# Kernel tuning notes

Measured on AMD Instinct MI355X. Metric: run time of the kernel, lower is better.

## Reference

```python
import jax, jax.numpy as jnp
import numpy as np

FORGET_BIAS = 1.0  # BasicLSTMCell default


def setup_inputs() -> dict:
    key = jax.random.key(0)
    k1, k2 = jax.random.split(key)
    B, T, F, H = 64, 128, 1024, 1024
    x = jax.random.normal(k1, (B, T, F), dtype=jnp.float32)
    # BasicLSTMCell kernel: [F + H, 4H], init uniform(-0.1, 0.1); bias zeros
    W = jax.random.uniform(k2, (F + H, 4 * H), dtype=jnp.float32, minval=-0.1, maxval=0.1)
    b = jnp.zeros((4 * H,), dtype=jnp.float32)
    return {"x": x, "W": W, "b": b}


def reference(x, W, b):
    # x: [B, T, F]; W: [F+H, 4H]; b: [4H]
    B, T, F = x.shape
    H = W.shape[1] // 4

    def step(carry, xt):
        c, h = carry  # [B, H] each
        z = jnp.concatenate([xt, h], axis=-1) @ W + b  # [B, 4H]
        i, j, f, o = jnp.split(z, 4, axis=-1)
        new_c = c * jax.nn.sigmoid(f + FORGET_BIAS) + jax.nn.sigmoid(i) * jnp.tanh(j)
        new_h = jnp.tanh(new_c) * jax.nn.sigmoid(o)
        return (new_c, new_h), new_h

    c0 = jnp.zeros((B, H), dtype=x.dtype)
    h0 = jnp.zeros((B, H), dtype=x.dtype)
    xs = jnp.swapaxes(x, 0, 1)  # [T, B, F]
    _, ys = jax.lax.scan(step, (c0, h0), xs)  # ys: [T, B, H]
    return jnp.swapaxes(ys, 0, 1)  # [B, T, H] (return_last=False, return_seq_2d=False)
```

## Files before the change

kernel.cpp:

```cpp
#include <hip/hip_runtime.h>
#include <stdint.h>

#define BATCH 64
#define TSEQ  128
#define FDIM  1024
#define HDIM  1024
#define GDIM  4096
#define MROWS 8192
#define NB    128

typedef short bf16x8 __attribute__((ext_vector_type(8)));
typedef float f32x4  __attribute__((ext_vector_type(4)));

__device__ __forceinline__ unsigned short f2bf(float f) {
    union { float f; uint32_t u; } v; v.f = f;
    uint32_t u = v.u;
    return (unsigned short)((u + 0x7FFFu + ((u >> 16) & 1u)) >> 16);
}
__device__ __forceinline__ float bf2f(unsigned short h) {
    union { uint32_t u; float f; } v; v.u = ((uint32_t)h) << 16; return v.f;
}
__device__ __forceinline__ float sigmoidf_(float x) { return 1.f / (1.f + __expf(-x)); }
__device__ __forceinline__ float tanhf_(float x)    { return 2.f / (1.f + __expf(-2.f * x)) - 1.f; }

union SP { short s[8]; int4 v; };
union UU { int4 i; bf16x8 v; };

__device__ __forceinline__ void st64cc(void* p, unsigned long long v) {
    __hip_atomic_store((unsigned long long*)p, v, __ATOMIC_RELAXED, __HIP_MEMORY_SCOPE_AGENT);
}
__device__ __forceinline__ void st32cc(void* p, uint32_t v) {
    __hip_atomic_store((uint32_t*)p, v, __ATOMIC_RELAXED, __HIP_MEMORY_SCOPE_AGENT);
}
__device__ __forceinline__ void gl16(const unsigned short* g, short* l) {
    __builtin_amdgcn_global_load_lds((const __attribute__((address_space(1))) void*)g,
                                     (__attribute__((address_space(3))) void*)l, 16, 0, 0);
}

__global__ void k_init(uint32_t* p, int nwords) {
    int i = blockIdx.x * blockDim.x + threadIdx.x;
    int s = gridDim.x * blockDim.x;
    for (; i < nwords; i += s) p[i] = 0;
}

__global__ __launch_bounds__(256) void k_cx(const float* __restrict__ x,
                                            unsigned short* __restrict__ xh,
                                            unsigned short* __restrict__ xl) {
    const int i = (blockIdx.x * 256 + threadIdx.x) * 16;
    float v[16];
    *(float4*)(v)      = *(const float4*)(x + i);
    *(float4*)(v + 4)  = *(const float4*)(x + i + 4);
    *(float4*)(v + 8)  = *(const float4*)(x + i + 8);
    *(float4*)(v + 12) = *(const float4*)(x + i + 12);
    SP h0, h1, l0, l1;
#pragma unroll
    for (int j = 0; j < 8; j++) {
        unsigned short h = f2bf(v[j]);
        h0.s[j] = (short)h; l0.s[j] = (short)f2bf(v[j] - bf2f(h));
        unsigned short g = f2bf(v[8 + j]);
        h1.s[j] = (short)g; l1.s[j] = (short)f2bf(v[8 + j] - bf2f(g));
    }
    *(int4*)(xh + i)     = h0.v;
    *(int4*)(xh + i + 8) = h1.v;
    *(int4*)(xl + i)     = l0.v;
    *(int4*)(xl + i + 8) = l1.v;
}

__global__ void k_tw(const float* __restrict__ W,
                     unsigned short* __restrict__ wxth, unsigned short* __restrict__ wxtl,
                     unsigned short* __restrict__ wht) {
    __shared__ float tile[64 * 65];
    const int nb = blockIdx.x;
    const int kb = blockIdx.y;
    const int t  = threadIdx.x;
    const int col = t & 63, rg = t >> 6;
#pragma unroll
    for (int i = 0; i < 16; i++) {
        int row = rg * 16 + i;
        tile[row * 65 + col] = W[(size_t)(kb * 64 + row) * 4096 + nb * 64 + col];
    }
    __syncthreads();
    if (kb < 16) {
        const int kbase = kb * 64;
#pragma unroll
        for (int i = 0; i < 16; i++) {
            int rp = rg * 16 + i;
            float v = tile[col * 65 + rp];
            unsigned short h = f2bf(v);
            size_t idx = (size_t)(nb * 64 + rp) * 1024 + kbase + col;
            wxth[idx] = h;
            wxtl[idx] = f2bf(v - bf2f(h));
        }
    } else {
        const int kbase = (kb - 16) * 64;
#pragma unroll
        for (int i = 0; i < 16; i++) {
            int rp = rg * 16 + i;
            float v = tile[col * 65 + rp];
            wht[(size_t)(nb * 64 + rp) * 1024 + kbase + col] = f2bf(v);
        }
    }
}

__global__ __launch_bounds__(256) void k_gemm1(const unsigned short* __restrict__ Xh,
                                               const unsigned short* __restrict__ Xl,
                                               const unsigned short* __restrict__ WxTh,
                                               const unsigned short* __restrict__ WxTl,
                                               float* __restrict__ xz) {
    __shared__ short Ash[128 * 32];
    __shared__ short Asl[128 * 32];
    __shared__ short Bsh[128 * 32];
    __shared__ short Bsl[128 * 32];
    const int n0 = blockIdx.x * 128;
    const int m0 = blockIdx.y * 128;
    const int t = threadIdx.x;
    const int wave = t >> 6, lane = t & 63;
    const int wm = wave >> 1, wn = wave & 1;
    const int q = lane >> 4, cl = lane & 15;

    const unsigned short* gsrc;
    short* lbase;
    if (wave == 0)      { gsrc = Xh   + (size_t)m0 * 1024; lbase = Ash; }
    else if (wave == 1) { gsrc = Xl   + (size_t)m0 * 1024; lbase = Asl; }
    else if (wave == 2) { gsrc = WxTh + (size_t)n0 * 1024; lbase = Bsh; }
    else                { gsrc = WxTl + (size_t)n0 * 1024; lbase = Bsl; }
    const unsigned short* gl_ptr = gsrc + (size_t)(lane >> 2) * 1024 + (lane & 3) * 8;

    f32x4 acc[4][4];
#pragma unroll
    for (int i = 0; i < 4; i++)
#pragma unroll
        for (int j = 0; j < 4; j++) acc[i][j] = (f32x4){0.f, 0.f, 0.f, 0.f};

    for (int kb = 0; kb < 32; kb++) {
        const int k0 = kb * 32;
        __syncthreads();
#pragma unroll
        for (int s = 0; s < 8; s++)
            gl16(gl_ptr + (size_t)s * 16 * 1024 + k0, lbase + s * 512);
        __syncthreads();
        bf16x8 ah[4], al[4], bh[4], bl[4];
#pragma unroll
        for (int i = 0; i < 4; i++) {
            ah[i] = *(const bf16x8*)(Ash + (wm * 64 + i * 16 + cl) * 32 + q * 8);
            al[i] = *(const bf16x8*)(Asl + (wm * 64 + i * 16 + cl) * 32 + q * 8);
        }
#pragma unroll
        for (int j = 0; j < 4; j++) {
            bh[j] = *(const bf16x8*)(Bsh + (wn * 64 + j * 16 + cl) * 32 + q * 8);
            bl[j] = *(const bf16x8*)(Bsl + (wn * 64 + j * 16 + cl) * 32 + q * 8);
        }
#pragma unroll
        for (int i = 0; i < 4; i++)
#pragma unroll
            for (int j = 0; j < 4; j++) {
                acc[i][j] = __builtin_amdgcn_mfma_f32_16x16x32_bf16(ah[i], bh[j], acc[i][j], 0, 0, 0);
                acc[i][j] = __builtin_amdgcn_mfma_f32_16x16x32_bf16(al[i], bh[j], acc[i][j], 0, 0, 0);
                acc[i][j] = __builtin_amdgcn_mfma_f32_16x16x32_bf16(ah[i], bl[j], acc[i][j], 0, 0, 0);
            }
    }
#pragma unroll
    for (int i = 0; i < 4; i++) {
#pragma unroll
        for (int j = 0; j < 4; j++) {
            int gm = m0 + wm * 64 + i * 16 + q * 4;
            int gn = n0 + wn * 64 + j * 16 + cl;
#pragma unroll
            for (int r = 0; r < 4; r++)
                xz[(size_t)(gm + r) * 4096 + gn] = acc[i][j][r];
        }
    }
}

__global__ __launch_bounds__(256) void k_gemm1_legacy(const float* __restrict__ Xf,
                                                      const unsigned short* __restrict__ WxTh,
                                                      const unsigned short* __restrict__ WxTl,
                                                      float* __restrict__ xz) {
    __shared__ short Ash[128 * 40];
    __shared__ short Asl[128 * 40];
    __shared__ short Bsh[128 * 40];
    __shared__ short Bsl[128 * 40];
    const int n0 = blockIdx.x * 128;
    const int m0 = blockIdx.y * 128;
    const int t = threadIdx.x;
    const int wave = t >> 6, lane = t & 63;
    const int wm = wave >> 1, wn = wave & 1;
    const int q = lane >> 4, cl = lane & 15;
    const int row_a = t >> 2;
    const int kc = (t & 3) * 8;

    f32x4 acc[4][4];
#pragma unroll
    for (int i = 0; i < 4; i++)
#pragma unroll
        for (int j = 0; j < 4; j++) acc[i][j] = (f32x4){0.f, 0.f, 0.f, 0.f};

    for (int kb = 0; kb < 32; kb++) {
        const int k0 = kb * 32;
        float va0[8], va1[8];
        {
            const float* p0 = Xf + (size_t)(m0 + row_a) * 1024 + k0 + kc;
            const float* p1 = Xf + (size_t)(m0 + 64 + row_a) * 1024 + k0 + kc;
            *(float4*)(va0)     = *(const float4*)(p0);
            *(float4*)(va0 + 4) = *(const float4*)(p0 + 4);
            *(float4*)(va1)     = *(const float4*)(p1);
            *(float4*)(va1 + 4) = *(const float4*)(p1 + 4);
        }
        int4 bh0 = *(const int4*)(WxTh + (size_t)(n0 + row_a)      * 1024 + k0 + kc);
        int4 bh1 = *(const int4*)(WxTh + (size_t)(n0 + 64 + row_a) * 1024 + k0 + kc);
        int4 bl0 = *(const int4*)(WxTl + (size_t)(n0 + row_a)      * 1024 + k0 + kc);
        int4 bl1 = *(const int4*)(WxTl + (size_t)(n0 + 64 + row_a) * 1024 + k0 + kc);
        __syncthreads();
        {
            SP h0, l0, h1, l1;
#pragma unroll
            for (int i = 0; i < 8; i++) {
                unsigned short h = f2bf(va0[i]);
                h0.s[i] = (short)h; l0.s[i] = (short)f2bf(va0[i] - bf2f(h));
                unsigned short g = f2bf(va1[i]);
                h1.s[i] = (short)g; l1.s[i] = (short)f2bf(va1[i] - bf2f(g));
            }
            *(int4*)(Ash + row_a * 40 + kc)        = h0.v;
            *(int4*)(Asl + row_a * 40 + kc)        = l0.v;
            *(int4*)(Ash + (64 + row_a) * 40 + kc) = h1.v;
            *(int4*)(Asl + (64 + row_a) * 40 + kc) = l1.v;
        }
        *(int4*)(Bsh + row_a * 40 + kc)        = bh0;
        *(int4*)(Bsh + (64 + row_a) * 40 + kc) = bh1;
        *(int4*)(Bsl + row_a * 40 + kc)        = bl0;
        *(int4*)(Bsl + (64 + row_a) * 40 + kc) = bl1;
        __syncthreads();
        bf16x8 ah[4], al[4], bh[4], bl[4];
#pragma unroll
        for (int i = 0; i < 4; i++) {
            ah[i] = *(const bf16x8*)(Ash + (wm * 64 + i * 16 + cl) * 40 + q * 8);
            al[i] = *(const bf16x8*)(Asl + (wm * 64 + i * 16 + cl) * 40 + q * 8);
        }
#pragma unroll
        for (int j = 0; j < 4; j++) {
            bh[j] = *(const bf16x8*)(Bsh + (wn * 64 + j * 16 + cl) * 40 + q * 8);
            bl[j] = *(const bf16x8*)(Bsl + (wn * 64 + j * 16 + cl) * 40 + q * 8);
        }
#pragma unroll
        for (int i = 0; i < 4; i++)
#pragma unroll
            for (int j = 0; j < 4; j++) {
                acc[i][j] = __builtin_amdgcn_mfma_f32_16x16x32_bf16(ah[i], bh[j], acc[i][j], 0, 0, 0);
                acc[i][j] = __builtin_amdgcn_mfma_f32_16x16x32_bf16(al[i], bh[j], acc[i][j], 0, 0, 0);
                acc[i][j] = __builtin_amdgcn_mfma_f32_16x16x32_bf16(ah[i], bl[j], acc[i][j], 0, 0, 0);
            }
    }
#pragma unroll
    for (int i = 0; i < 4; i++) {
#pragma unroll
        for (int j = 0; j < 4; j++) {
            int gm = m0 + wm * 64 + i * 16 + q * 4;
            int gn = n0 + wn * 64 + j * 16 + cl;
#pragma unroll
            for (int r = 0; r < 4; r++)
                xz[(size_t)(gm + r) * 4096 + gn] = acc[i][j][r];
        }
    }
}

__global__ __launch_bounds__(256, 1) void k_rnn(const float* __restrict__ xz,
                                                const unsigned short* __restrict__ WhT,
                                                const float* __restrict__ bias,
                                                unsigned short* hrot,
                                                int* flags,
                                                float* __restrict__ out) {
    __shared__ short hs[64 * 8];
    const int t = threadIdx.x;
    const int blk = blockIdx.x;
    const int n0 = (((blk & 7) << 4) | (blk >> 3)) * 8;
    const int wave = t >> 6, lane = t & 63;
    const int q = lane >> 4, cl = lane & 15;
    const int m = wave * 16 + cl;

    const int cc = cl & 7;
    const bool act = (cl < 8);
    float bi = 0.f, bj = 0.f, bfv = 0.f, bo = 0.f;
    if (act) {
        bi  = bias[n0 + cc];
        bj  = bias[1024 + n0 + cc];
        bfv = bias[2048 + n0 + cc];
        bo  = bias[3072 + n0 + cc];
    }

    bf16x8 B0[32], B1[32];
    {
        const unsigned short* bsrc0 =
            WhT + (size_t)((cl >> 3) * 1024 + n0 + (cl & 7)) * 1024 + q * 8;
        const unsigned short* bsrc1 =
            WhT + (size_t)((2 + (cl >> 3)) * 1024 + n0 + (cl & 7)) * 1024 + q * 8;
#pragma unroll
        for (int kb = 0; kb < 32; kb++) {
            UU u0, u1;
            u0.i = *(const int4*)(bsrc0 + kb * 32);
            u1.i = *(const int4*)(bsrc1 + kb * 32);
            B0[kb] = u0.v;
            B1[kb] = u1.v;
        }
    }

    float c[4] = {0.f, 0.f, 0.f, 0.f};
    const unsigned long long selfmask =
        ((t & 63) == (blk >> 1)) ? ((blk & 1) ? (1ULL << 32) : 1ULL) : 0ULL;

    for (int tt = 0; tt < TSEQ; tt++) {
        float pxi[4], pxj[4], pxf[4], pxo[4];
        if (act) {
#pragma unroll
            for (int r = 0; r < 4; r++) {
                int m2 = wave * 16 + q * 4 + r;
                const float* xp = xz + (size_t)(m2 * 128 + tt) * 4096 + n0 + cc;
                pxi[r] = xp[0];
                pxj[r] = xp[1024];
                pxf[r] = xp[2048];
                pxo[r] = xp[3072];
            }
        }
        __builtin_amdgcn_sched_barrier(0);
        if (tt > 0) {
            if (t < 64) {
                const unsigned long long* fp =
                    (const unsigned long long*)flags + (size_t)(tt - 1) * 64 + t;
                unsigned long long v;
                do {
                    v = __hip_atomic_load(fp, __ATOMIC_RELAXED, __HIP_MEMORY_SCOPE_AGENT);
                } while (!__all((v | selfmask) == 0x0000000100000001ULL));
            }
            __syncthreads();
        }
        const char* ab = (const char*)hrot + (size_t)tt * 131072 + (size_t)m * 2048 + q * 16;
        UU aa[32];
#pragma unroll
        for (int kb = 0; kb < 32; kb++) aa[kb].i = *(const int4*)(ab + kb * 64);
        __builtin_amdgcn_sched_barrier(0);

        f32x4 acc0a = (f32x4){0.f, 0.f, 0.f, 0.f};
        f32x4 acc0b = (f32x4){0.f, 0.f, 0.f, 0.f};
        f32x4 acc1a = (f32x4){0.f, 0.f, 0.f, 0.f};
        f32x4 acc1b = (f32x4){0.f, 0.f, 0.f, 0.f};
#pragma unroll
        for (int kb = 0; kb < 32; kb += 2) {
            acc0a = __builtin_amdgcn_mfma_f32_16x16x32_bf16(aa[kb].v,     B0[kb],     acc0a, 0, 0, 0);
            acc1a = __builtin_amdgcn_mfma_f32_16x16x32_bf16(aa[kb].v,     B1[kb],     acc1a, 0, 0, 0);
            acc0b = __builtin_amdgcn_mfma_f32_16x16x32_bf16(aa[kb + 1].v, B0[kb + 1], acc0b, 0, 0, 0);
            acc1b = __builtin_amdgcn_mfma_f32_16x16x32_bf16(aa[kb + 1].v, B1[kb + 1], acc1b, 0, 0, 0);
        }
        f32x4 acc0 = acc0a + acc0b;
        f32x4 acc1 = acc1a + acc1b;
        float zi[4], zj[4], zf[4], zo[4];
#pragma unroll
        for (int r = 0; r < 4; r++) {
            float a0 = acc0[r], a1 = acc1[r];
            float a0x = __shfl_xor(a0, 8);
            float a1x = __shfl_xor(a1, 8);
            zi[r] = a0; zj[r] = a0x; zf[r] = a1; zo[r] = a1x;
        }
        float hv4[4];
        if (act) {
#pragma unroll
            for (int r = 0; r < 4; r++) {
                float vi = zi[r] + pxi[r] + bi;
                float vj = zj[r] + pxj[r] + bj;
                float vf = zf[r] + pxf[r] + bfv + 1.0f;
                float vo = zo[r] + pxo[r] + bo;
                float cn = c[r] * sigmoidf_(vf) + sigmoidf_(vi) * tanhf_(vj);
                c[r] = cn;
                float h = tanhf_(cn) * sigmoidf_(vo);
                hv4[r] = h;
                hs[(wave * 16 + q * 4 + r) * 8 + cc] = (short)f2bf(h);
            }
        }
        __syncthreads();
        if (t < 128) {
            unsigned long long hv = *(const unsigned long long*)(hs + (t >> 1) * 8 + (t & 1) * 4);
            st64cc((char*)hrot + (size_t)(tt + 1) * 131072 + (size_t)(t >> 1) * 2048 + n0 * 2 + (t & 1) * 8, hv);
        }
        __syncthreads();
        if (t == 0) st32cc(flags + (size_t)tt * NB + blk, 1u);
        if (act) {
#pragma unroll
            for (int r = 0; r < 4; r++) {
                int m2 = wave * 16 + q * 4 + r;
                out[(size_t)(m2 * 128 + tt) * 1024 + n0 + cc] = hv4[r];
            }
        }
    }
}

extern "C" void kernel_launch(void* const* d_in, const int* in_sizes, int n_in,
                              void* d_out, int out_size, void* d_ws, size_t ws_size,
                              hipStream_t stream) {
    const float* x = (const float*)d_in[0];
    const float* W = (const float*)d_in[1];
    const float* b = (const float*)d_in[2];
    float* out = (float*)d_out;
    char* ws = (char*)d_ws;

    unsigned short* WXTH = (unsigned short*)(ws);
    unsigned short* WXTL = (unsigned short*)(ws + (size_t)8  * 1024 * 1024);
    unsigned short* WHT  = (unsigned short*)(ws + (size_t)16 * 1024 * 1024);
    float*          XZ   = (float*)         (ws + (size_t)24 * 1024 * 1024);
    int*            FLAGS= (int*)           (ws + (size_t)152 * 1024 * 1024);
    unsigned short* HROT = (unsigned short*)(ws + (size_t)152 * 1024 * 1024 + 65536);
    unsigned short* XH   = (unsigned short*)(ws + (size_t)170 * 1024 * 1024);
    unsigned short* XL   = (unsigned short*)(ws + (size_t)186 * 1024 * 1024);
    const int use_pre = (ws_size >= (size_t)202 * 1024 * 1024) ? 1 : 0;

    k_init<<<256, 256, 0, stream>>>((uint32_t*)FLAGS, 49152);
    dim3 gtw(64, 32);
    k_tw<<<gtw, 256, 0, stream>>>(W, WXTH, WXTL, WHT);
    dim3 gg(32, 64);
    if (use_pre) {
        k_cx<<<2048, 256, 0, stream>>>(x, XH, XL);
        k_gemm1<<<gg, 256, 0, stream>>>(XH, XL, WXTH, WXTL, XZ);
    } else {
        k_gemm1_legacy<<<gg, 256, 0, stream>>>(x, WXTH, WXTL, XZ);
    }
    k_rnn<<<NB, 256, 0, stream>>>(XZ, WHT, b, HROT, FLAGS, out);
}
```

Before: 1.025 ms.

## Fuse input-projection GEMM with recurrent LSTM kernel via per-tile ready flags

Merges the input-projection GEMM and the persistent recurrent kernel into one launch. The first 128 blocks run the recurrence and the remaining 2048 blocks compute GEMM tiles. GEMM rows are remapped so each tile covers two timesteps for all batch rows, letting the recurrence start as soon as early timesteps are ready instead of waiting for the whole GEMM. Readiness is signalled through global flags that recurrent blocks poll. The change depends on the 128 recurrent blocks being resident together with the GEMM blocks and adds polling overhead, and the GEMM now writes with a strided row pattern.

```diff
diff --git a/kernel.cpp b/kernel.cpp
--- a/kernel.cpp
+++ b/kernel.cpp
@@ -8,6 +8,7 @@
 #define GDIM  4096
 #define MROWS 8192
 #define NB    128
+#define GBLK  2048
 
 typedef short bf16x8 __attribute__((ext_vector_type(8)));
 typedef float f32x4  __attribute__((ext_vector_type(4)));
@@ -102,72 +103,235 @@
     }
 }
 
-__global__ __launch_bounds__(256) void k_gemm1(const unsigned short* __restrict__ Xh,
-                                               const unsigned short* __restrict__ Xl,
-                                               const unsigned short* __restrict__ WxTh,
-                                               const unsigned short* __restrict__ WxTl,
-                                               float* __restrict__ xz) {
-    __shared__ short Ash[128 * 32];
-    __shared__ short Asl[128 * 32];
-    __shared__ short Bsh[128 * 32];
-    __shared__ short Bsl[128 * 32];
-    const int n0 = blockIdx.x * 128;
-    const int m0 = blockIdx.y * 128;
+__global__ __launch_bounds__(256, 1) void k_fused(
+        const unsigned short* __restrict__ Xh, const unsigned short* __restrict__ Xl,
+        const unsigned short* __restrict__ WxTh, const unsigned short* __restrict__ WxTl,
+        float* __restrict__ xz,
+        const unsigned short* __restrict__ WhT, const float* __restrict__ bias,
+        unsigned short* hrot,
+        int* flags,
+        int* gflags,
+        float* __restrict__ out) {
+    __shared__ short Sh[16384];
+    __shared__ short hs[64 * 8];
     const int t = threadIdx.x;
     const int wave = t >> 6, lane = t & 63;
-    const int wm = wave >> 1, wn = wave & 1;
     const int q = lane >> 4, cl = lane & 15;
 
-    const unsigned short* gsrc;
-    short* lbase;
-    if (wave == 0)      { gsrc = Xh   + (size_t)m0 * 1024; lbase = Ash; }
-    else if (wave == 1) { gsrc = Xl   + (size_t)m0 * 1024; lbase = Asl; }
-    else if (wave == 2) { gsrc = WxTh + (size_t)n0 * 1024; lbase = Bsh; }
-    else                { gsrc = WxTl + (size_t)n0 * 1024; lbase = Bsl; }
-    const unsigned short* gl_ptr = gsrc + (size_t)(lane >> 2) * 1024 + (lane & 3) * 8;
-
-    f32x4 acc[4][4];
-#pragma unroll
-    for (int i = 0; i < 4; i++)
-#pragma unroll
-        for (int j = 0; j < 4; j++) acc[i][j] = (f32x4){0.f, 0.f, 0.f, 0.f};
-
-    for (int kb = 0; kb < 32; kb++) {
-        const int k0 = kb * 32;
-        __syncthreads();
-#pragma unroll
-        for (int s = 0; s < 8; s++)
-            gl16(gl_ptr + (size_t)s * 16 * 1024 + k0, lbase + s * 512);
-        __syncthreads();
-        bf16x8 ah[4], al[4], bh[4], bl[4];
+    if (blockIdx.x >= NB) {
+        const int bid2 = blockIdx.x - NB;
+        const int bx = bid2 & 31, by = bid2 >> 5;
+        const int n0g = bx * 128;
+        const int wm = wave >> 1, wn = wave & 1;
+        short* Ash = Sh;
+        short* Asl = Sh + 4096;
+        short* Bsh = Sh + 8192;
+        short* Bsl = Sh + 12288;
+        const unsigned short* gA;
+        short* lb;
+        if (wave == 0)      { gA = Xh; lb = Ash; }
+        else if (wave == 1) { gA = Xl; lb = Asl; }
+        else if (wave == 2) { gA = WxTh + (size_t)n0g * 1024; lb = Bsh; }
+        else                { gA = WxTl + (size_t)n0g * 1024; lb = Bsl; }
+        const int kcg = (lane & 3) * 8;
+        const int rb = lane >> 2;
+
+        f32x4 acc[4][4];
+#pragma unroll
+        for (int i = 0; i < 4; i++)
+#pragma unroll
+            for (int j = 0; j < 4; j++) acc[i][j] = (f32x4){0.f, 0.f, 0.f, 0.f};
+
+        for (int kb = 0; kb < 32; kb++) {
+            const int k0 = kb * 32;
+            __syncthreads();
+#pragma unroll
+            for (int s = 0; s < 8; s++) {
+                const int r = rb + s * 16;
+                size_t grow;
+                if (wave < 2) grow = (size_t)((r & 63) * 128 + 2 * by + (r >> 6));
+                else          grow = (size_t)r;
+                gl16(gA + grow * 1024 + k0 + kcg, lb + s * 512);
+            }
+            __syncthreads();
+            bf16x8 ah[4], al[4], bh[4], bl[4];
+#pragma unroll
+            for (int i = 0; i < 4; i++) {
+                ah[i] = *(const bf16x8*)(Ash + (wm * 64 + i * 16 + cl) * 32 + q * 8);
+                al[i] = *(const bf16x8*)(Asl + (wm * 64 + i * 16 + cl) * 32 + q * 8);
+            }
+#pragma unroll
+            for (int j = 0; j < 4; j++) {
+                bh[j] = *(const bf16x8*)(Bsh + (wn * 64 + j * 16 + cl) * 32 + q * 8);
+                bl[j] = *(const bf16x8*)(Bsl + (wn * 64 + j * 16 + cl) * 32 + q * 8);
+            }
+#pragma unroll
+            for (int i = 0; i < 4; i++)
+#pragma unroll
+                for (int j = 0; j < 4; j++) {
+                    acc[i][j] = __builtin_amdgcn_mfma_f32_16x16x32_bf16(ah[i], bh[j], acc[i][j], 0, 0, 0);
+                    acc[i][j] = __builtin_amdgcn_mfma_f32_16x16x32_bf16(al[i], bh[j], acc[i][j], 0, 0, 0);
+                    acc[i][j] = __builtin_amdgcn_mfma_f32_16x16x32_bf16(ah[i], bl[j], acc[i][j], 0, 0, 0);
+                }
+        }
 #pragma unroll
         for (int i = 0; i < 4; i++) {
-            ah[i] = *(const bf16x8*)(Ash + (wm * 64 + i * 16 + cl) * 32 + q * 8);
-            al[i] = *(const bf16x8*)(Asl + (wm * 64 + i * 16 + cl) * 32 + q * 8);
-        }
-#pragma unroll
-        for (int j = 0; j < 4; j++) {
-            bh[j] = *(const bf16x8*)(Bsh + (wn * 64 + j * 16 + cl) * 32 + q * 8);
-            bl[j] = *(const bf16x8*)(Bsl + (wn * 64 + j * 16 + cl) * 32 + q * 8);
-        }
-#pragma unroll
-        for (int i = 0; i < 4; i++)
 #pragma unroll
             for (int j = 0; j < 4; j++) {
-                acc[i][j] = __builtin_amdgcn_mfma_f32_16x16x32_bf16(ah[i], bh[j], acc[i][j], 0, 0, 0);
-                acc[i][j] = __builtin_amdgcn_mfma_f32_16x16x32_bf16(al[i], bh[j], acc[i][j], 0, 0, 0);
-                acc[i][j] = __builtin_amdgcn_mfma_f32_16x16x32_bf16(ah[i], bl[j], acc[i][j], 0, 0, 0);
-            }
-    }
-#pragma unroll
-    for (int i = 0; i < 4; i++) {
-#pragma unroll
-        for (int j = 0; j < 4; j++) {
-            int gm = m0 + wm * 64 + i * 16 + q * 4;
-            int gn = n0 + wn * 64 + j * 16 + cl;
-#pragma unroll
-            for (int r = 0; r < 4; r++)
-                xz[(size_t)(gm + r) * 4096 + gn] = acc[i][j][r];
+                const int tr = wm * 64 + i * 16 + q * 4;
+                const int gn = n0g + wn * 64 + j * 16 + cl;
+#pragma unroll
+                for (int r2 = 0; r2 < 4; r2++) {
+                    const int rr = tr + r2;
+                    const size_t grow = (size_t)((rr & 63) * 128 + 2 * by + (rr >> 6));
+                    st32cc(xz + grow * 4096 + gn, __float_as_uint(acc[i][j][r2]));
+                }
+            }
+        }
+        asm volatile("s_waitcnt vmcnt(0)" ::: "memory");
+        __syncthreads();
+        if (t == 0) st32cc(gflags + by * 32 + bx, 1u);
+        return;
+    }
+
+    const int blk = blockIdx.x;
+    const int n0 = (((blk & 7) << 4) | (blk >> 3)) * 8;
+    const int m = wave * 16 + cl;
+
+    const int cc = cl & 7;
+    const bool act = (cl < 8);
+    float bi = 0.f, bj = 0.f, bfv = 0.f, bo = 0.f;
+    if (act) {
+        bi  = bias[n0 + cc];
+        bj  = bias[1024 + n0 + cc];
+        bfv = bias[2048 + n0 + cc];
+        bo  = bias[3072 + n0 + cc];
+    }
+
+    bf16x8 B0[32], B1[32];
+    {
+        const unsigned short* bsrc0 =
+            WhT + (size_t)((cl >> 3) * 1024 + n0 + (cl & 7)) * 1024 + q * 8;
+        const unsigned short* bsrc1 =
+            WhT + (size_t)((2 + (cl >> 3)) * 1024 + n0 + (cl & 7)) * 1024 + q * 8;
+#pragma unroll
+        for (int kb = 0; kb < 32; kb++) {
+            UU u0, u1;
+            u0.i = *(const int4*)(bsrc0 + kb * 32);
+            u1.i = *(const int4*)(bsrc1 + kb * 32);
+            B0[kb] = u0.v;
+            B1[kb] = u1.v;
+        }
+    }
+
+    float c[4] = {0.f, 0.f, 0.f, 0.f};
+    const unsigned long long selfmask =
+        ((t & 63) == (blk >> 1)) ? ((blk & 1) ? (1ULL << 32) : 1ULL) : 0ULL;
+
+    if (wave == 1) {
+        bool ok;
+        do {
+            unsigned long long v = (lane < 4)
+                ? __hip_atomic_load((const unsigned long long*)gflags + lane,
+                                    __ATOMIC_RELAXED, __HIP_MEMORY_SCOPE_AGENT)
+                : 0x0000000100000001ULL;
+            ok = (v == 0x0000000100000001ULL);
+        } while (!__all(ok));
+    }
+    __syncthreads();
+
+    for (int tt = 0; tt < TSEQ; tt++) {
+        float pxi[4], pxj[4], pxf[4], pxo[4];
+        if (act) {
+#pragma unroll
+            for (int r = 0; r < 4; r++) {
+                int m2 = wave * 16 + q * 4 + r;
+                const float* xp = xz + (size_t)(m2 * 128 + tt) * 4096 + n0 + cc;
+                pxi[r] = xp[0];
+                pxj[r] = xp[1024];
+                pxf[r] = xp[2048];
+                pxo[r] = xp[3072];
+            }
+        }
+        __builtin_amdgcn_sched_barrier(0);
+        if (tt > 0) {
+            if (t < 64) {
+                const unsigned long long* fp =
+                    (const unsigned long long*)flags + (size_t)(tt - 1) * 64 + t;
+                unsigned long long v;
+                do {
+                    v = __hip_atomic_load(fp, __ATOMIC_RELAXED, __HIP_MEMORY_SCOPE_AGENT);
+                } while (!__all((v | selfmask) == 0x0000000100000001ULL));
+            } else if (wave == 1) {
+                const int byn = (tt + 2) >> 1;
+                if (byn < 64) {
+                    bool ok;
+                    do {
+                        unsigned long long v = (lane < 4)
+                            ? __hip_atomic_load((const unsigned long long*)gflags + byn * 4 + lane,
+                                                __ATOMIC_RELAXED, __HIP_MEMORY_SCOPE_AGENT)
+                            : 0x0000000100000001ULL;
+                        ok = (v == 0x0000000100000001ULL);
+                    } while (!__all(ok));
+                }
+            }
+            __syncthreads();
+        }
+        const char* ab = (const char*)hrot + (size_t)tt * 131072 + (size_t)m * 2048 + q * 16;
+        UU aa[32];
+#pragma unroll
+        for (int kb = 0; kb < 32; kb++) aa[kb].i = *(const int4*)(ab + kb * 64);
+        __builtin_amdgcn_sched_barrier(0);
+
+        f32x4 acc0a = (f32x4){0.f, 0.f, 0.f, 0.f};
+        f32x4 acc0b = (f32x4){0.f, 0.f, 0.f, 0.f};
+        f32x4 acc1a = (f32x4){0.f, 0.f, 0.f, 0.f};
+        f32x4 acc1b = (f32x4){0.f, 0.f, 0.f, 0.f};
+#pragma unroll
+        for (int kb = 0; kb < 32; kb += 2) {
+            acc0a = __builtin_amdgcn_mfma_f32_16x16x32_bf16(aa[kb].v,     B0[kb],     acc0a, 0, 0, 0);
+            acc1a = __builtin_amdgcn_mfma_f32_16x16x32_bf16(aa[kb].v,     B1[kb],     acc1a, 0, 0, 0);
+            acc0b = __builtin_amdgcn_mfma_f32_16x16x32_bf16(aa[kb + 1].v, B0[kb + 1], acc0b, 0, 0, 0);
+            acc1b = __builtin_amdgcn_mfma_f32_16x16x32_bf16(aa[kb + 1].v, B1[kb + 1], acc1b, 0, 0, 0);
+        }
+        f32x4 acc0 = acc0a + acc0b;
+        f32x4 acc1 = acc1a + acc1b;
+        float zi[4], zj[4], zf[4], zo[4];
+#pragma unroll
+        for (int r = 0; r < 4; r++) {
+            float a0 = acc0[r], a1 = acc1[r];
+            float a0x = __shfl_xor(a0, 8);
+            float a1x = __shfl_xor(a1, 8);
+            zi[r] = a0; zj[r] = a0x; zf[r] = a1; zo[r] = a1x;
+        }
+        float hv4[4];
+        if (act) {
+#pragma unroll
+            for (int r = 0; r < 4; r++) {
+                float vi = zi[r] + pxi[r] + bi;
+                float vj = zj[r] + pxj[r] + bj;
+                float vf = zf[r] + pxf[r] + bfv + 1.0f;
+                float vo = zo[r] + pxo[r] + bo;
+                float cn = c[r] * sigmoidf_(vf) + sigmoidf_(vi) * tanhf_(vj);
+                c[r] = cn;
+                float h = tanhf_(cn) * sigmoidf_(vo);
+                hv4[r] = h;
+                hs[(wave * 16 + q * 4 + r) * 8 + cc] = (short)f2bf(h);
+            }
+        }
+        __syncthreads();
+        if (t < 128) {
+            unsigned long long hv = *(const unsigned long long*)(hs + (t >> 1) * 8 + (t & 1) * 4);
+            st64cc((char*)hrot + (size_t)(tt + 1) * 131072 + (size_t)(t >> 1) * 2048 + n0 * 2 + (t & 1) * 8, hv);
+        }
+        __syncthreads();
+        if (t == 0) st32cc(flags + (size_t)tt * NB + blk, 1u);
+        if (act) {
+#pragma unroll
+            for (int r = 0; r < 4; r++) {
+                int m2 = wave * 16 + q * 4 + r;
+                out[(size_t)(m2 * 128 + tt) * 1024 + n0 + cc] = hv4[r];
+            }
         }
     }
 }
@@ -286,7 +450,6 @@
         bfv = bias[2048 + n0 + cc];
         bo  = bias[3072 + n0 + cc];
     }
-
     bf16x8 B0[32], B1[32];
     {
         const unsigned short* bsrc0 =
@@ -302,7 +465,6 @@
             B1[kb] = u1.v;
         }
     }
-
     float c[4] = {0.f, 0.f, 0.f, 0.f};
     const unsigned long long selfmask =
         ((t & 63) == (blk >> 1)) ? ((blk & 1) ? (1ULL << 32) : 1ULL) : 0ULL;
@@ -405,20 +567,22 @@
     unsigned short* WHT  = (unsigned short*)(ws + (size_t)16 * 1024 * 1024);
     float*          XZ   = (float*)         (ws + (size_t)24 * 1024 * 1024);
     int*            FLAGS= (int*)           (ws + (size_t)152 * 1024 * 1024);
-    unsigned short* HROT = (unsigned short*)(ws + (size_t)152 * 1024 * 1024 + 65536);
+    int*            GFLAGS=(int*)           (ws + (size_t)152 * 1024 * 1024 + 65536);
+    unsigned short* HROT = (unsigned short*)(ws + (size_t)152 * 1024 * 1024 + 131072);
     unsigned short* XH   = (unsigned short*)(ws + (size_t)170 * 1024 * 1024);
     unsigned short* XL   = (unsigned short*)(ws + (size_t)186 * 1024 * 1024);
     const int use_pre = (ws_size >= (size_t)202 * 1024 * 1024) ? 1 : 0;
 
-    k_init<<<256, 256, 0, stream>>>((uint32_t*)FLAGS, 49152);
+    k_init<<<256, 256, 0, stream>>>((uint32_t*)FLAGS, 65536);
     dim3 gtw(64, 32);
     k_tw<<<gtw, 256, 0, stream>>>(W, WXTH, WXTL, WHT);
-    dim3 gg(32, 64);
     if (use_pre) {
         k_cx<<<2048, 256, 0, stream>>>(x, XH, XL);
-        k_gemm1<<<gg, 256, 0, stream>>>(XH, XL, WXTH, WXTL, XZ);
+        k_fused<<<NB + GBLK, 256, 0, stream>>>(XH, XL, WXTH, WXTL, XZ, WHT, b,
+                                               HROT, FLAGS, GFLAGS, out);
     } else {
+        dim3 gg(32, 64);
         k_gemm1_legacy<<<gg, 256, 0, stream>>>(x, WXTH, WXTL, XZ);
-    }
-    k_rnn<<<NB, 256, 0, stream>>>(XZ, WHT, b, HROT, FLAGS, out);
-}
+        k_rnn<<<NB, 256, 0, stream>>>(XZ, WHT, b, HROT, FLAGS, out);
+    }
+}
```

Measured after the change: 895.5 us. 1.14x faster.
